# Optimization experiments

Hardware: AMD Instinct MI355X
Metric: run time of the kernel (lower is better)

## Reference

```python
import jax, jax.numpy as jnp
import numpy as np

B, LQ, LV = 32, 64, 128
QS, FS, BN = 512, 1024, 512

def setup_inputs() -> dict:
    key = jax.random.key(0)
    k1, k2, k3, k4, k5 = jax.random.split(key, 5)
    s = lambda n: 1.0 / np.sqrt(n)
    return {
        "phr_feats": jax.random.normal(k1, (B, LQ, QS), dtype=jnp.float32),
        "vis_feats": jax.random.normal(k2, (B, LV, FS), dtype=jnp.float32),
        "W": jax.random.uniform(k3, (BN, QS), jnp.float32, -s(QS), s(QS)),
        "U": jax.random.uniform(k4, (BN, FS), jnp.float32, -s(FS), s(FS)),
        "b": jnp.ones((BN,), dtype=jnp.float32),
        "w": jax.random.uniform(k5, (1, BN), jnp.float32, -s(BN), s(BN)),
    }

def reference(phr_feats, vis_feats, W, U, b, w):
    # Wh: [B,Lq,BN], Uv: [B,Lv,BN]
    Wh = jnp.einsum('bqd,nd->bqn', phr_feats, W)
    Uv = jnp.einsum('bvf,nf->bvn', vis_feats, U)
    # broadcast add + tanh: [B,Lq,Lv,BN]
    t = jnp.tanh(Wh[:, :, None, :] + Uv[:, None, :, :] + b)
    energies = jnp.einsum('bqvn,n->bqv', t, w[0])  # squeeze(-1)
    weights = jax.nn.softmax(energies, axis=2)
    aligned = jnp.einsum('bqv,bvf->bqf', weights, vis_feats)
    semantic_group_feats = jnp.concatenate([phr_feats, aligned], axis=2)
    return (semantic_group_feats, weights, energies)
```

## Files before the change

kernel.cpp:

```cpp
#include <hip/hip_runtime.h>

#define NB  32
#define NLQ 64
#define NLV 128
#define NQS 512
#define NFS 1024
#define NBN 512
#define CC  2.8853900817779268f

typedef float  floatx4 __attribute__((ext_vector_type(4)));
typedef __bf16 bf16x8  __attribute__((ext_vector_type(8)));
typedef unsigned short us;

__device__ __forceinline__ us f2bf(float f) {
    unsigned int u = __float_as_uint(f);
    u += 0x7fffu + ((u >> 16) & 1u);
    return (us)(u >> 16);
}
__device__ __forceinline__ unsigned int pktrunc(float lo, float hi) {
    return __builtin_amdgcn_perm(__float_as_uint(hi), __float_as_uint(lo), 0x07060302u);
}
__device__ __forceinline__ float blo(unsigned int u) {
    return __uint_as_float(u << 16);
}
__device__ __forceinline__ float bhi(unsigned int u) {
    return __uint_as_float(u & 0xffff0000u);
}

__device__ __forceinline__ void gemm64(
    us* As, us* Bs,
    const float* __restrict__ A, const float* __restrict__ Bt,
    const float* __restrict__ bias,
    float* __restrict__ whYp, us* __restrict__ uvYTp,
    int K, int bx, int by, float* __restrict__ sgf)
{
    const int tid  = threadIdx.x;
    const int m0   = bx * 64;
    const int n0   = by * 64;
    const int wave = tid >> 6;
    const int lane = tid & 63;
    const int wm   = (wave >> 1) * 32;
    const int wn   = (wave & 1) * 32;
    const int srow = tid >> 2;
    const int sk   = (tid & 3) * 8;
    const int fm   = lane & 15;
    const int fko  = (lane >> 4) * 8;

    floatx4 acc[2][2] = {};
    const float* ag = A  + (size_t)(m0 + srow) * K + sk;
    const float* bg = Bt + (size_t)(n0 + srow) * K + sk;

    float4 a0 = *(const float4*)(ag),     a1 = *(const float4*)(ag + 4);
    float4 b0 = *(const float4*)(bg),     b1 = *(const float4*)(bg + 4);

    for (int k0 = 0; k0 < K; k0 += 32) {
        __syncthreads();
        if (sgf) {
            float* d = sgf + (size_t)(m0 + srow) * (NQS + NFS) + k0 + sk;
            *(float4*)d       = a0;
            *(float4*)(d + 4) = a1;
        }
        uint4 av = { pktrunc(a0.x, a0.y), pktrunc(a0.z, a0.w),
                     pktrunc(a1.x, a1.y), pktrunc(a1.z, a1.w) };
        uint4 bv = { pktrunc(b0.x, b0.y), pktrunc(b0.z, b0.w),
                     pktrunc(b1.x, b1.y), pktrunc(b1.z, b1.w) };
        *(uint4*)(As + srow * 40 + sk) = av;
        *(uint4*)(Bs + srow * 40 + sk) = bv;
        const int kn = k0 + 32;
        if (kn < K) {
            a0 = *(const float4*)(ag + kn); a1 = *(const float4*)(ag + kn + 4);
            b0 = *(const float4*)(bg + kn); b1 = *(const float4*)(bg + kn + 4);
        }
        __syncthreads();
        bf16x8 am[2], bn[2];
        #pragma unroll
        for (int i = 0; i < 2; ++i)
            am[i] = *(const bf16x8*)(As + (wm + 16 * i + fm) * 40 + fko);
        #pragma unroll
        for (int j = 0; j < 2; ++j)
            bn[j] = *(const bf16x8*)(Bs + (wn + 16 * j + fm) * 40 + fko);
        #pragma unroll
        for (int i = 0; i < 2; ++i)
            #pragma unroll
            for (int j = 0; j < 2; ++j)
                acc[i][j] = __builtin_amdgcn_mfma_f32_16x16x32_bf16(am[i], bn[j], acc[i][j], 0, 0, 0);
    }

    const int cr = (lane >> 4) * 4;
    const int cc = lane & 15;
    if (whYp) {
        #pragma unroll
        for (int j = 0; j < 2; ++j) {
            int gn = n0 + wn + 16 * j + cc;
            float bj = bias[gn];
            #pragma unroll
            for (int i = 0; i < 2; ++i)
                #pragma unroll
                for (int r = 0; r < 4; ++r) {
                    int gm = m0 + wm + 16 * i + cr + r;
                    whYp[(size_t)gm * NBN + gn] =
                        __builtin_amdgcn_exp2f(CC * (acc[i][j][r] + bj));
                }
        }
    } else {
        #pragma unroll
        for (int i = 0; i < 2; ++i)
            #pragma unroll
            for (int j = 0; j < 2; ++j) {
                int gm0 = m0 + wm + 16 * i + cr;
                int gn  = n0 + wn + 16 * j + cc;
                int bb  = gm0 >> 7, v0 = gm0 & 127;
                unsigned int y0 = f2bf(__builtin_amdgcn_exp2f(CC * acc[i][j][0]));
                unsigned int y1 = f2bf(__builtin_amdgcn_exp2f(CC * acc[i][j][1]));
                unsigned int y2 = f2bf(__builtin_amdgcn_exp2f(CC * acc[i][j][2]));
                unsigned int y3 = f2bf(__builtin_amdgcn_exp2f(CC * acc[i][j][3]));
                uint2 pk2 = { y0 | (y1 << 16), y2 | (y3 << 16) };
                *(uint2*)(uvYTp + ((size_t)bb * NBN + gn) * NLV + v0) = pk2;
            }
    }
}

__global__ __launch_bounds__(256) void gemm_both(
    const float* __restrict__ phr, const float* __restrict__ W,
    const float* __restrict__ bias,
    const float* __restrict__ vis, const float* __restrict__ U,
    float* __restrict__ whY, us* __restrict__ uvYT,
    float* __restrict__ out_sgf)
{
    __shared__ __align__(16) us As[64 * 40];
    __shared__ __align__(16) us Bs[64 * 40];
    int blk = blockIdx.x;
    if (blk < 256) {
        int bx = blk % 32, by = blk / 32;
        gemm64(As, Bs, phr, W, bias, whY, nullptr, NQS, bx, by,
               by == 0 ? out_sgf : nullptr);
    } else {
        blk -= 256;
        int bx = blk % 64, by = blk / 64;
        gemm64(As, Bs, vis, U, bias, nullptr, uvYT, NFS, bx, by, nullptr);
    }
}

__global__ __launch_bounds__(256) void energize(
    const float* __restrict__ whY,
    const us* __restrict__ uvYT,
    const float* __restrict__ wvec,
    float* __restrict__ out_w, float* __restrict__ out_e,
    us* __restrict__ p_bf, us* __restrict__ p_lo)
{
    const float LOG2E = 1.4426950408889634f;
    int blk = blockIdx.x;
    blk = (blk & 7) * 64 + (blk >> 3);
    const int b    = blk >> 4;
    const int qq4  = blk & 15;
    const int tid  = threadIdx.x;
    const int wave = __builtin_amdgcn_readfirstlane(tid >> 6);
    const int lane = tid & 63;
    const int q0   = qq4 * 4;

    __shared__ float part[4][4][NLV];

    float4 sw0 = *(const float4*)(wvec + lane * 8);
    float4 sw1 = *(const float4*)(wvec + lane * 8 + 4);
    float sumw = sw0.x + sw0.y + sw0.z + sw0.w + sw1.x + sw1.y + sw1.z + sw1.w;
    #pragma unroll
    for (int off = 32; off; off >>= 1) sumw += __shfl_xor(sumw, off);

    const float* yqp = whY + (size_t)(b * NLQ + q0) * NBN + wave * 128;
    const float* wp  = wvec + wave * 128;
    const us*    uvp = uvYT + ((size_t)b * NBN + wave * 128) * NLV + 2 * lane;

    float acc[4][2] = {};
    #pragma unroll 2
    for (int nc = 0; nc < 128; nc += 8) {
        unsigned int yv[8];
        #pragma unroll
        for (int k = 0; k < 8; ++k)
            yv[k] = *(const unsigned int*)(uvp + (size_t)(nc + k) * NLV);
        #pragma unroll
        for (int k = 0; k < 8; ++k) {
            float x0 = blo(yv[k]), x1 = bhi(yv[k]);
            float wk = wp[nc + k];
            #pragma unroll
            for (int q = 0; q < 4; ++q) {
                float yq = yqp[q * NBN + nc + k];
                float d0 = fmaf(x0, yq, 1.f);
                float d1 = fmaf(x1, yq, 1.f);
                acc[q][0] = fmaf(wk, __builtin_amdgcn_rcpf(d0), acc[q][0]);
                acc[q][1] = fmaf(wk, __builtin_amdgcn_rcpf(d1), acc[q][1]);
            }
        }
    }
    #pragma unroll
    for (int q = 0; q < 4; ++q) {
        float2 t = { acc[q][0], acc[q][1] };
        *(float2*)&part[q][wave][2 * lane] = t;
    }
    __syncthreads();

    const int q = wave;
    float s0 = 0.f, s1 = 0.f;
    #pragma unroll
    for (int nq = 0; nq < 4; ++nq) {
        s0 += part[q][nq][2 * lane];
        s1 += part[q][nq][2 * lane + 1];
    }
    float e0 = sumw - 2.f * s0;
    float e1 = sumw - 2.f * s1;
    float m = fmaxf(e0, e1);
    #pragma unroll
    for (int off = 32; off; off >>= 1) m = fmaxf(m, __shfl_xor(m, off));
    float x0 = __builtin_amdgcn_exp2f((e0 - m) * LOG2E);
    float x1 = __builtin_amdgcn_exp2f((e1 - m) * LOG2E);
    float ss = x0 + x1;
    #pragma unroll
    for (int off = 32; off; off >>= 1) ss += __shfl_xor(ss, off);
    float inv = __builtin_amdgcn_rcpf(ss);
    float p0 = x0 * inv, p1 = x1 * inv;

    const size_t row = (size_t)(b * NLQ + q0 + q);
    float2 ep = { e0, e1 };
    float2 pp = { p0, p1 };
    *(float2*)(out_e + row * NLV + 2 * lane) = ep;
    *(float2*)(out_w + row * NLV + 2 * lane) = pp;
    unsigned int pb0 = f2bf(p0), pb1 = f2bf(p1);
    float lo0 = p0 - __uint_as_float(pb0 << 16);
    float lo1 = p1 - __uint_as_float(pb1 << 16);
    unsigned int lb0 = f2bf(lo0), lb1 = f2bf(lo1);
    *(unsigned int*)(p_bf + row * NLV + 2 * lane) = pb0 | (pb1 << 16);
    *(unsigned int*)(p_lo + row * NLV + 2 * lane) = lb0 | (lb1 << 16);
}

__global__ __launch_bounds__(256) void aligned_mfma(
    const us* __restrict__ p_bf, const us* __restrict__ p_lo,
    const float* __restrict__ vis,
    float* __restrict__ out_sgf)
{
    int blk = blockIdx.x;
    blk = (blk & 7) * 64 + (blk >> 3);
    const int b    = blk >> 4;
    const int ft   = blk & 15;
    const int tid  = threadIdx.x;
    const int wave = tid >> 6;
    const int lane = tid & 63;
    const int wm   = (wave >> 1) * 32;
    const int wf   = (wave & 1) * 32;
    const int fm   = lane & 15;
    const int fko  = (lane >> 4) * 8;

    __shared__ us Vs[64][136];

    {
        const int v  = tid >> 1;
        const int fh = (tid & 1) * 32;
        const float* vp = vis + ((size_t)b * NLV + v) * NFS + ft * 64 + fh;
        #pragma unroll
        for (int r = 0; r < 8; ++r) {
            float4 x = ((const float4*)vp)[r];
            Vs[fh + 4 * r + 0][v] = (us)(__float_as_uint(x.x) >> 16);
            Vs[fh + 4 * r + 1][v] = (us)(__float_as_uint(x.y) >> 16);
            Vs[fh + 4 * r + 2][v] = (us)(__float_as_uint(x.z) >> 16);
            Vs[fh + 4 * r + 3][v] = (us)(__float_as_uint(x.w) >> 16);
        }
    }
    __syncthreads();

    floatx4 acc[2][2] = {};
    const us* pA  = p_bf + ((size_t)b * NLQ + wm + fm) * NLV + fko;
    const us* pAl = p_lo + ((size_t)b * NLQ + wm + fm) * NLV + fko;

    #pragma unroll
    for (int ks = 0; ks < 4; ++ks) {
        bf16x8 a[2], al[2], bb2[2];
        #pragma unroll
        for (int i = 0; i < 2; ++i) {
            a[i]  = *(const bf16x8*)(pA  + (size_t)i * 16 * NLV + ks * 32);
            al[i] = *(const bf16x8*)(pAl + (size_t)i * 16 * NLV + ks * 32);
        }
        #pragma unroll
        for (int j = 0; j < 2; ++j)
            bb2[j] = *(const bf16x8*)&Vs[wf + 16 * j + fm][ks * 32 + fko];
        #pragma unroll
        for (int i = 0; i < 2; ++i)
            #pragma unroll
            for (int j = 0; j < 2; ++j) {
                acc[i][j] = __builtin_amdgcn_mfma_f32_16x16x32_bf16(a[i],  bb2[j], acc[i][j], 0, 0, 0);
                acc[i][j] = __builtin_amdgcn_mfma_f32_16x16x32_bf16(al[i], bb2[j], acc[i][j], 0, 0, 0);
            }
    }

    const int cr = (lane >> 4) * 4;
    const int cc = lane & 15;
    #pragma unroll
    for (int i = 0; i < 2; ++i)
        #pragma unroll
        for (int j = 0; j < 2; ++j)
            #pragma unroll
            for (int r = 0; r < 4; ++r) {
                int q = wm + 16 * i + cr + r;
                int f = ft * 64 + wf + 16 * j + cc;
                size_t row = (size_t)b * NLQ + q;
                out_sgf[row * (NQS + NFS) + NQS + f] = acc[i][j][r];
            }
}

extern "C" void kernel_launch(void* const* d_in, const int* in_sizes, int n_in,
                              void* d_out, int out_size, void* d_ws, size_t ws_size,
                              hipStream_t stream) {
    const float* phr  = (const float*)d_in[0];
    const float* vis  = (const float*)d_in[1];
    const float* W    = (const float*)d_in[2];
    const float* U    = (const float*)d_in[3];
    const float* bias = (const float*)d_in[4];
    const float* wvec = (const float*)d_in[5];

    char* ws = (char*)d_ws;
    float* whY  = (float*)ws;
    us* uvYT    = (us*)(ws + (4u << 20));
    us* p_bf    = (us*)(ws + (8u << 20));
    us* p_lo    = (us*)(ws + (8u << 20) + (512u << 10));

    float* out     = (float*)d_out;
    float* out_sgf = out;
    float* out_w   = out_sgf + (size_t)NB * NLQ * (NQS + NFS);
    float* out_e   = out_w   + (size_t)NB * NLQ * NLV;

    gemm_both<<<768, 256, 0, stream>>>(phr, W, bias, vis, U, whY, uvYT, out_sgf);
    energize<<<512, 256, 0, stream>>>(whY, uvYT, wvec, out_w, out_e, p_bf, p_lo);
    aligned_mfma<<<512, 256, 0, stream>>>(p_bf, p_lo, vis, out_sgf);
}
```

Baseline: 126.3 us.

## Pair reciprocals in energize, double its waves, stage uvYT stores through LDS

The energize kernel now combines two w/(1+xy) terms over a common denominator, so it needs one reciprocal per pair of hidden units instead of two. It also launches 512 threads per block, giving each of 8 waves 64 hidden units, and reduces 8 partial sums. The transposed bf16 store of Uv in the GEMM now goes through shared memory so global writes are 16-byte coalesced rows. The trade-off is more multiplies and some risk of overflow or precision loss in the product of denominators, plus extra barriers and LDS traffic in the GEMM epilogue.

```diff
diff --git a/kernel.cpp b/kernel.cpp
--- a/kernel.cpp
+++ b/kernel.cpp
@@ -28,12 +28,14 @@
 }
 
 __device__ __forceinline__ void gemm64(
-    us* As, us* Bs,
+    us* smem,
     const float* __restrict__ A, const float* __restrict__ Bt,
     const float* __restrict__ bias,
     float* __restrict__ whYp, us* __restrict__ uvYTp,
     int K, int bx, int by, float* __restrict__ sgf)
 {
+    us* As = smem;
+    us* Bs = smem + 64 * 40;
     const int tid  = threadIdx.x;
     const int m0   = bx * 64;
     const int n0   = by * 64;
@@ -103,20 +105,29 @@
                 }
         }
     } else {
+        us* Cs = smem;
+        __syncthreads();
         #pragma unroll
         for (int i = 0; i < 2; ++i)
             #pragma unroll
             for (int j = 0; j < 2; ++j) {
-                int gm0 = m0 + wm + 16 * i + cr;
-                int gn  = n0 + wn + 16 * j + cc;
-                int bb  = gm0 >> 7, v0 = gm0 & 127;
-                unsigned int y0 = f2bf(__builtin_amdgcn_exp2f(CC * acc[i][j][0]));
-                unsigned int y1 = f2bf(__builtin_amdgcn_exp2f(CC * acc[i][j][1]));
-                unsigned int y2 = f2bf(__builtin_amdgcn_exp2f(CC * acc[i][j][2]));
-                unsigned int y3 = f2bf(__builtin_amdgcn_exp2f(CC * acc[i][j][3]));
-                uint2 pk2 = { y0 | (y1 << 16), y2 | (y3 << 16) };
-                *(uint2*)(uvYTp + ((size_t)bb * NBN + gn) * NLV + v0) = pk2;
+                int nl = wn + 16 * j + cc;
+                int vl = wm + 16 * i + cr;
+                #pragma unroll
+                for (int r = 0; r < 4; ++r)
+                    Cs[nl * 72 + vl + r] =
+                        f2bf(__builtin_amdgcn_exp2f(CC * acc[i][j][r]));
             }
+        __syncthreads();
+        const int bb    = m0 >> 7;
+        const int vbase = m0 & 127;
+        const int nl    = tid >> 2;
+        const int vc    = (tid & 3) * 16;
+        uint4 t0 = *(const uint4*)(Cs + nl * 72 + vc);
+        uint4 t1 = *(const uint4*)(Cs + nl * 72 + vc + 8);
+        us* dst = uvYTp + ((size_t)bb * NBN + n0 + nl) * NLV + vbase + vc;
+        *(uint4*)dst       = t0;
+        *(uint4*)(dst + 8) = t1;
     }
 }
 
@@ -127,21 +138,20 @@
     float* __restrict__ whY, us* __restrict__ uvYT,
     float* __restrict__ out_sgf)
 {
-    __shared__ __align__(16) us As[64 * 40];
-    __shared__ __align__(16) us Bs[64 * 40];
+    __shared__ __align__(16) us smem[2 * 64 * 40];
     int blk = blockIdx.x;
     if (blk < 256) {
         int bx = blk % 32, by = blk / 32;
-        gemm64(As, Bs, phr, W, bias, whY, nullptr, NQS, bx, by,
+        gemm64(smem, phr, W, bias, whY, nullptr, NQS, bx, by,
                by == 0 ? out_sgf : nullptr);
     } else {
         blk -= 256;
         int bx = blk % 64, by = blk / 64;
-        gemm64(As, Bs, vis, U, bias, nullptr, uvYT, NFS, bx, by, nullptr);
-    }
-}
-
-__global__ __launch_bounds__(256) void energize(
+        gemm64(smem, vis, U, bias, nullptr, uvYT, NFS, bx, by, nullptr);
+    }
+}
+
+__global__ __launch_bounds__(512) void energize(
     const float* __restrict__ whY,
     const us* __restrict__ uvYT,
     const float* __restrict__ wvec,
@@ -158,7 +168,7 @@
     const int lane = tid & 63;
     const int q0   = qq4 * 4;
 
-    __shared__ float part[4][4][NLV];
+    __shared__ float part[4][8][NLV];
 
     float4 sw0 = *(const float4*)(wvec + lane * 8);
     float4 sw1 = *(const float4*)(wvec + lane * 8 + 4);
@@ -166,28 +176,33 @@
     #pragma unroll
     for (int off = 32; off; off >>= 1) sumw += __shfl_xor(sumw, off);
 
-    const float* yqp = whY + (size_t)(b * NLQ + q0) * NBN + wave * 128;
-    const float* wp  = wvec + wave * 128;
-    const us*    uvp = uvYT + ((size_t)b * NBN + wave * 128) * NLV + 2 * lane;
+    const float* yqp = whY + (size_t)(b * NLQ + q0) * NBN + wave * 64;
+    const float* wp  = wvec + wave * 64;
+    const us*    uvp = uvYT + ((size_t)b * NBN + wave * 64) * NLV + 2 * lane;
 
     float acc[4][2] = {};
     #pragma unroll 2
-    for (int nc = 0; nc < 128; nc += 8) {
+    for (int nc = 0; nc < 64; nc += 8) {
         unsigned int yv[8];
         #pragma unroll
         for (int k = 0; k < 8; ++k)
             yv[k] = *(const unsigned int*)(uvp + (size_t)(nc + k) * NLV);
         #pragma unroll
-        for (int k = 0; k < 8; ++k) {
-            float x0 = blo(yv[k]), x1 = bhi(yv[k]);
-            float wk = wp[nc + k];
+        for (int kk = 0; kk < 4; ++kk) {
+            const int k0 = nc + 2 * kk, k1 = k0 + 1;
+            float x0a = blo(yv[2 * kk]),     x0b = bhi(yv[2 * kk]);
+            float x1a = blo(yv[2 * kk + 1]), x1b = bhi(yv[2 * kk + 1]);
+            float w0 = wp[k0], w1 = wp[k1];
             #pragma unroll
             for (int q = 0; q < 4; ++q) {
-                float yq = yqp[q * NBN + nc + k];
-                float d0 = fmaf(x0, yq, 1.f);
-                float d1 = fmaf(x1, yq, 1.f);
-                acc[q][0] = fmaf(wk, __builtin_amdgcn_rcpf(d0), acc[q][0]);
-                acc[q][1] = fmaf(wk, __builtin_amdgcn_rcpf(d1), acc[q][1]);
+                float y0 = yqp[q * NBN + k0];
+                float y1 = yqp[q * NBN + k1];
+                float d0a = fmaf(x0a, y0, 1.f), d1a = fmaf(x1a, y1, 1.f);
+                float d0b = fmaf(x0b, y0, 1.f), d1b = fmaf(x1b, y1, 1.f);
+                float numa = fmaf(w0, d1a, w1 * d0a);
+                float numb = fmaf(w0, d1b, w1 * d0b);
+                acc[q][0] = fmaf(numa, __builtin_amdgcn_rcpf(d0a * d1a), acc[q][0]);
+                acc[q][1] = fmaf(numb, __builtin_amdgcn_rcpf(d0b * d1b), acc[q][1]);
             }
         }
     }
@@ -198,37 +213,39 @@
     }
     __syncthreads();
 
-    const int q = wave;
-    float s0 = 0.f, s1 = 0.f;
-    #pragma unroll
-    for (int nq = 0; nq < 4; ++nq) {
-        s0 += part[q][nq][2 * lane];
-        s1 += part[q][nq][2 * lane + 1];
-    }
-    float e0 = sumw - 2.f * s0;
-    float e1 = sumw - 2.f * s1;
-    float m = fmaxf(e0, e1);
-    #pragma unroll
-    for (int off = 32; off; off >>= 1) m = fmaxf(m, __shfl_xor(m, off));
-    float x0 = __builtin_amdgcn_exp2f((e0 - m) * LOG2E);
-    float x1 = __builtin_amdgcn_exp2f((e1 - m) * LOG2E);
-    float ss = x0 + x1;
-    #pragma unroll
-    for (int off = 32; off; off >>= 1) ss += __shfl_xor(ss, off);
-    float inv = __builtin_amdgcn_rcpf(ss);
-    float p0 = x0 * inv, p1 = x1 * inv;
-
-    const size_t row = (size_t)(b * NLQ + q0 + q);
-    float2 ep = { e0, e1 };
-    float2 pp = { p0, p1 };
-    *(float2*)(out_e + row * NLV + 2 * lane) = ep;
-    *(float2*)(out_w + row * NLV + 2 * lane) = pp;
-    unsigned int pb0 = f2bf(p0), pb1 = f2bf(p1);
-    float lo0 = p0 - __uint_as_float(pb0 << 16);
-    float lo1 = p1 - __uint_as_float(pb1 << 16);
-    unsigned int lb0 = f2bf(lo0), lb1 = f2bf(lo1);
-    *(unsigned int*)(p_bf + row * NLV + 2 * lane) = pb0 | (pb1 << 16);
-    *(unsigned int*)(p_lo + row * NLV + 2 * lane) = lb0 | (lb1 << 16);
+    if (wave < 4) {
+        const int q = wave;
+        float s0 = 0.f, s1 = 0.f;
+        #pragma unroll
+        for (int nq = 0; nq < 8; ++nq) {
+            s0 += part[q][nq][2 * lane];
+            s1 += part[q][nq][2 * lane + 1];
+        }
+        float e0 = sumw - 2.f * s0;
+        float e1 = sumw - 2.f * s1;
+        float m = fmaxf(e0, e1);
+        #pragma unroll
+        for (int off = 32; off; off >>= 1) m = fmaxf(m, __shfl_xor(m, off));
+        float x0 = __builtin_amdgcn_exp2f((e0 - m) * LOG2E);
+        float x1 = __builtin_amdgcn_exp2f((e1 - m) * LOG2E);
+        float ss = x0 + x1;
+        #pragma unroll
+        for (int off = 32; off; off >>= 1) ss += __shfl_xor(ss, off);
+        float inv = __builtin_amdgcn_rcpf(ss);
+        float p0 = x0 * inv, p1 = x1 * inv;
+
+        const size_t row = (size_t)(b * NLQ + q0 + q);
+        float2 ep = { e0, e1 };
+        float2 pp = { p0, p1 };
+        *(float2*)(out_e + row * NLV + 2 * lane) = ep;
+        *(float2*)(out_w + row * NLV + 2 * lane) = pp;
+        unsigned int pb0 = f2bf(p0), pb1 = f2bf(p1);
+        float lo0 = p0 - __uint_as_float(pb0 << 16);
+        float lo1 = p1 - __uint_as_float(pb1 << 16);
+        unsigned int lb0 = f2bf(lo0), lb1 = f2bf(lo1);
+        *(unsigned int*)(p_bf + row * NLV + 2 * lane) = pb0 | (pb1 << 16);
+        *(unsigned int*)(p_lo + row * NLV + 2 * lane) = lb0 | (lb1 << 16);
+    }
 }
 
 __global__ __launch_bounds__(256) void aligned_mfma(
@@ -326,6 +343,6 @@
     float* out_e   = out_w   + (size_t)NB * NLQ * NLV;
 
     gemm_both<<<768, 256, 0, stream>>>(phr, W, bias, vis, U, whY, uvYT, out_sgf);
-    energize<<<512, 256, 0, stream>>>(whY, uvYT, wvec, out_w, out_e, p_bf, p_lo);
+    energize<<<512, 512, 0, stream>>>(whY, uvYT, wvec, out_w, out_e, p_bf, p_lo);
     aligned_mfma<<<512, 256, 0, stream>>>(p_bf, p_lo, vis, out_sgf);
 }
```

New measurement: 124.9 us. Within noise of the previous version (-1.1%).
